# Optimization experiments

Hardware: AMD Instinct MI355X
Metric: run time of the kernel (lower is better)

Reference implementation:

```python
import jax, jax.numpy as jnp
import numpy as np

BETA = 1.0
EPS_MU = 1e-6
EPS_LOG = 1e-8
D_DIM = 2048
M_EVENTS = 16384
T_HORIZON = 100


def setup_inputs() -> dict:
    key = jax.random.key(0)
    k1, k2 = jax.random.split(key)
    # sorted event times in [0, T_HORIZON)
    t_events = jnp.sort(jax.random.uniform(k1, (M_EVENTS,), jnp.float32) * T_HORIZON)
    marks = jax.random.randint(k2, (M_EVENTS,), 0, D_DIM)  # int marks in {0..D-1}
    # learned params, init exactly as in torch module
    log_mu = jnp.full((D_DIM,), -3.0, jnp.float32)
    log_alpha = jnp.full((D_DIM, D_DIM), -4.0, jnp.float32)
    return {
        "t_events": t_events,
        "marks": marks,
        "T_max": T_HORIZON,
        "log_mu": log_mu,
        "log_alpha": log_alpha,
    }


def _loglik(t_events, log_mu, log_alpha, marks, T_max, beta=BETA):
    mu = jax.nn.softplus(log_mu) + EPS_MU          # [D]
    alpha = jax.nn.softplus(log_alpha)             # [D, D]
    D = mu.shape[0]
    # dt[0] = 0 so the first step leaves S (= zeros) untouched, matching the
    # torch loop which skips decay at n == 0.
    dt = jnp.concatenate([jnp.zeros((1,), t_events.dtype), jnp.diff(t_events)])  # [M]

    def step(S, xs):
        dt_n, d = xs
        S = jnp.exp(-beta * dt_n) * S              # exponential decay of state [D]
        lam_d = mu[d] + alpha[d] @ S               # intensity at event's mark
        S = S.at[d].add(1.0)                       # self-excitation bump
        return S, jnp.log(lam_d + EPS_LOG)

    _, log_lams = jax.lax.scan(step, jnp.zeros((D,), mu.dtype), (dt, marks))

    # compensator integral term
    T = jnp.asarray(T_max, t_events.dtype)
    one_minus_exp = 1.0 - jnp.exp(-beta * (T - t_events))          # [M]
    contrib = jax.ops.segment_sum(one_minus_exp, marks, num_segments=D)  # [D]
    integral = mu * T + alpha @ (contrib / beta)                   # [D]
    return log_lams.sum() - integral.sum()


def reference(t_events, marks, T_max, log_mu, log_alpha):
    return _loglik(t_events, log_mu, log_alpha, marks, T_max)
```

## Files before the change

### kernel.cpp

```cpp
#include <hip/hip_runtime.h>
#include <math.h>

#define D_DIM 2048
#define M_EV  16384
#define LCH   32
#define CCH   (M_EV / LCH)
#define SEG   32
#define NSEG  (CCH / SEG)
#define EPSEG (SEG * LCH)
#define BETA  1.0f
#define CPB   8

__device__ __forceinline__ float softplus_f(float x){
  float e = __expf(-fabsf(x));
  return fmaxf(x, 0.0f) + __logf(1.0f + e);
}

__device__ __forceinline__ unsigned short f2bf(float f){
  unsigned b = __float_as_uint(f);
  return (unsigned short)((b + 0x7FFFu + ((b >> 16) & 1u)) >> 16);
}
__device__ __forceinline__ float bf2f(unsigned short u){
  return __uint_as_float(((unsigned)u) << 16);
}

__device__ __forceinline__ float decode_T(const void* p){
  unsigned bits = *(const unsigned*)p;
  float fv = __uint_as_float(bits);
  return (fv >= 1e-3f && fv <= 1e7f) ? fv : (float)(int)bits;
}

__device__ __forceinline__ float wave_red(float v){
  #pragma unroll
  for (int o = 32; o > 0; o >>= 1) v += __shfl_down(v, o);
  return v;
}

__global__ __launch_bounds__(256) void k_prep(
    const float* __restrict__ t, const int* __restrict__ m,
    const float* __restrict__ log_mu, const void* Tp,
    float* __restrict__ muw, float* __restrict__ Cpart,
    float* __restrict__ acc)
{
  __shared__ float Cl[D_DIM];
  __shared__ float red[4];
  const int b = blockIdx.x, tid = threadIdx.x;
  if (b < 8){
    int j = b*256 + tid;
    float v = softplus_f(log_mu[j]) + 1e-6f;
    muw[j] = v;
    float s = wave_red(v);
    if ((tid & 63) == 0) red[tid >> 6] = s;
    __syncthreads();
    if (tid == 0) acc[8 + b] = (red[0]+red[1]) + (red[2]+red[3]);
  } else if (b < 8 + CPB){
    float4* Cl4 = (float4*)Cl;
    const float4 z = make_float4(0.f,0.f,0.f,0.f);
    Cl4[tid*2] = z; Cl4[tid*2 + 1] = z;
    __syncthreads();
    const float T = decode_T(Tp);
    #pragma unroll
    for (int k = 0; k < 8; ++k){
      int i = (b-8)*2048 + k*256 + tid;
      atomicAdd(&Cl[m[i]], 1.0f - __expf(-BETA * (T - t[i])));
    }
    __syncthreads();
    float4* Cp4 = (float4*)(Cpart + (size_t)(b-8) * D_DIM);
    Cp4[tid*2]     = Cl4[tid*2];
    Cp4[tid*2 + 1] = Cl4[tid*2 + 1];
  } else {
    if (tid < 8) acc[tid] = 0.f;
  }
}

__global__ __launch_bounds__(256) void k_scan_alpha(
    const float* __restrict__ t, const int* __restrict__ m,
    float* __restrict__ SL, float* __restrict__ Carry,
    const float* __restrict__ la, const float* __restrict__ Cpart,
    unsigned short* __restrict__ sA, float* __restrict__ acc)
{
  __shared__ float Stile[SEG * 256];
  __shared__ float tec[SEG];
  __shared__ float dch[SEG];
  const int b = blockIdx.x, tid = threadIdx.x;
  if (b < 128){
    const int seg = b >> 3, jb = b & 7;
    {
      float4* S4 = (float4*)Stile;
      const float4 z = make_float4(0.f,0.f,0.f,0.f);
      #pragma unroll
      for (int k = 0; k < 8; ++k) S4[k*256 + tid] = z;
    }
    if (tid < SEG){
      int c = seg*SEG + tid;
      if (c < CCH-1){
        float te = t[(c+1)*LCH];
        tec[tid] = te;
        dch[tid] = __expf(t[c*LCH] - te);
      } else {
        tec[tid] = 0.f;
        dch[tid] = 1.0f;
      }
    }
    __syncthreads();
    #pragma unroll
    for (int e = 0; e < 4; ++e){
      int il = e*256 + tid;
      int i  = seg*EPSEG + il;
      int cl = il >> 5;
      int c  = seg*SEG + cl;
      int mk = m[i] - jb*256;
      if (c < CCH-1 && (unsigned)mk < 256u)
        atomicAdd(&Stile[cl*256 + mk], __expf(t[i] - tec[cl]));
    }
    __syncthreads();
    const int col = jb*256 + tid;
    float u = 0.f;
    #pragma unroll 4
    for (int cl = 0; cl < SEG; ++cl){
      int c = seg*SEG + cl;
      SL[(size_t)c * D_DIM + col] = u;
      u = fmaf(dch[cl], u, Stile[cl*256 + tid]);
    }
    Carry[(size_t)seg * D_DIM + col] = u;
    return;
  }
  const int nthreads = 512*256;
  int atid = (b-128)*256 + tid;
  const float4* Cp4 = (const float4*)Cpart;
  const int cq = atid & 511;
  float4 cb = make_float4(0.f,0.f,0.f,0.f);
  #pragma unroll
  for (int r = 0; r < CPB; ++r){
    float4 v = Cp4[r*512 + cq];
    cb.x += v.x; cb.y += v.y; cb.z += v.z; cb.w += v.w;
  }
  const float4* la4 = (const float4*)la;
  ushort4* sA4 = (ushort4*)sA;
  float p = 0.f;
  #pragma unroll
  for (int u = 0; u < 8; ++u){
    int i4 = atid + u * nthreads;
    float4 x = la4[i4];
    float4 sp;
    sp.x = softplus_f(x.x); sp.y = softplus_f(x.y);
    sp.z = softplus_f(x.z); sp.w = softplus_f(x.w);
    ushort4 h;
    h.x = f2bf(sp.x); h.y = f2bf(sp.y); h.z = f2bf(sp.z); h.w = f2bf(sp.w);
    sA4[i4] = h;
    p = fmaf(sp.x, cb.x, p);
    p = fmaf(sp.y, cb.y, p);
    p = fmaf(sp.z, cb.z, p);
    p = fmaf(sp.w, cb.w, p);
  }
  float w = wave_red(p);
  int lane = tid & 63, wid = tid >> 6;
  if (lane == 0) Stile[wid] = w;
  __syncthreads();
  if (tid == 0) atomicAdd(&acc[1], Stile[0]+Stile[1]+Stile[2]+Stile[3]);
}

__global__ __launch_bounds__(512) void k_events(
    const float* __restrict__ t, const int* __restrict__ m,
    const unsigned short* __restrict__ sA, const float* __restrict__ muw,
    const float* __restrict__ SL, const float* __restrict__ Carry,
    float* __restrict__ acc, const void* Tp, float* __restrict__ out){
  __shared__ float S0[D_DIM];
  __shared__ float tl[LCH];
  __shared__ int   ml[LCH];
  __shared__ float wred[8];
  __shared__ float asg[16];
  const int tid = threadIdx.x;
  const int c = blockIdx.x;
  const int seg = c >> 5;

  if (tid < LCH){
    ml[tid] = m[c*LCH + tid];
    tl[tid] = t[c*LCH + tid];
  } else if (tid >= 64 && tid < 64 + NSEG - 1){
    int s = tid - 64;
    asg[s] = __expf(t[s*EPSEG] - t[(s+1)*EPSEG]);
  }
  __syncthreads();

  {
    const float cd = __expf(t[seg*EPSEG] - tl[0]);
    const float4 sv = *(const float4*)(SL + (size_t)c * D_DIM + tid*4);
    float4 e = {0.f, 0.f, 0.f, 0.f};
    float wgt = 1.f;
    for (int s = seg - 1; s >= 0; --s){
      const float4 cr = *(const float4*)(Carry + (size_t)s * D_DIM + tid*4);
      e.x = fmaf(cr.x, wgt, e.x); e.y = fmaf(cr.y, wgt, e.y);
      e.z = fmaf(cr.z, wgt, e.z); e.w = fmaf(cr.w, wgt, e.w);
      wgt *= asg[s];
    }
    float4 s;
    s.x = fmaf(e.x, cd, sv.x); s.y = fmaf(e.y, cd, sv.y);
    s.z = fmaf(e.z, cd, sv.z); s.w = fmaf(e.w, cd, sv.w);
    *(float4*)&S0[tid*4] = s;
  }
  __syncthreads();

  const int l = tid & 63, w = tid >> 6;
  const int l4 = l * 4;

  float4 s0[8];
  #pragma unroll
  for (int u = 0; u < 8; ++u) s0[u] = *(const float4*)&S0[u*256 + l4];

  const float t0 = tl[0];
  float lgw = 0.f;
  #pragma unroll
  for (int q = 0; q < 4; ++q){
    const int k = w*4 + q;
    const int d = ml[k];
    const unsigned short* row = sA + (size_t)d * D_DIM;
    float p = 0.f;
    #pragma unroll
    for (int u = 0; u < 8; ++u){
      ushort4 a = *(const ushort4*)(row + u*256 + l4);
      p = fmaf(bf2f(a.x), s0[u].x, p);
      p = fmaf(bf2f(a.y), s0[u].y, p);
      p = fmaf(bf2f(a.z), s0[u].z, p);
      p = fmaf(bf2f(a.w), s0[u].w, p);
    }
    const float tk = tl[k];
    float g = 0.f;
    if (l < k) g = bf2f(row[ml[l]]) * __expf(tl[l] - tk);
    p = fmaf(p, __expf(t0 - tk), g);
    float v = wave_red(p);
    if (l == 0) lgw += __logf(muw[d] + v + 1e-8f);
  }
  if (l == 0) wred[w] = lgw;
  __syncthreads();
  if (tid == 0){
    float lg = ((wred[0]+wred[1])+(wred[2]+wred[3]))
             + ((wred[4]+wred[5])+(wred[6]+wred[7]));
    atomicAdd(&acc[0], lg);
    __threadfence();
    unsigned old = atomicAdd((unsigned*)&acc[3], 1u);
    if (old == CCH - 1){
      float a0 = atomicAdd(&acc[0], 0.0f);
      float a1 = atomicAdd(&acc[1], 0.0f);
      float musum = 0.f;
      #pragma unroll
      for (int j = 8; j < 16; ++j) musum += atomicAdd(&acc[j], 0.0f);
      float T = decode_T(Tp);
      out[0] = a0 - (T * musum + a1 * (1.0f / BETA));
    }
  }
}

extern "C" void kernel_launch(void* const* d_in, const int* in_sizes, int n_in,
                              void* d_out, int out_size, void* d_ws, size_t ws_size,
                              hipStream_t stream) {
  const float* t_events  = (const float*)d_in[0];
  const int*   marks     = (const int*)  d_in[1];
  const void*  Tp        =               d_in[2];
  const float* log_mu    = (const float*)d_in[3];
  const float* log_alpha = (const float*)d_in[4];
  float* out = (float*)d_out;

  float* ws      = (float*)d_ws;
  float* SL      = ws;
  float* Carry   = SL + (size_t)CCH * D_DIM;
  float* muw     = Carry + (size_t)NSEG * D_DIM;
  float* Cpart   = muw + D_DIM;
  float* acc     = Cpart + (size_t)CPB * D_DIM;
  unsigned short* sA = (unsigned short*)(acc + 16);

  k_prep      <<<17, 256, 0, stream>>>(t_events, marks, log_mu, Tp,
                                       muw, Cpart, acc);
  k_scan_alpha<<<640, 256, 0, stream>>>(t_events, marks, SL, Carry,
                                        log_alpha, Cpart, sA, acc);
  k_events    <<<CCH, 512, 0, stream>>>(t_events, marks, sA, muw, SL, Carry,
                                        acc, Tp, out);
}
```

Measured before the change: 113.4 us.

## Recompute in-segment prefix state in LDS instead of materializing per-chunk SL

Drops the per-chunk prefix-state array SL, which was 512 × 2048 floats written by the scan kernel and read back by the event kernel. Each event block now rebuilds its within-segment state by scattering the earlier events of its segment into shared memory with atomics, decayed to the chunk start. The segment carries move into extra blocks of the prep kernel, so the former scan/alpha kernel shrinks to just the alpha softplus and reduction. This trades several megabytes of global traffic for up to about 1000 LDS atomics per event block, which can contend on repeated marks.

Result: no change. 112.7 us (-0.6%).

```diff
diff --git a/kernel.cpp b/kernel.cpp
--- a/kernel.cpp
+++ b/kernel.cpp
@@ -40,7 +40,7 @@
     const float* __restrict__ t, const int* __restrict__ m,
     const float* __restrict__ log_mu, const void* Tp,
     float* __restrict__ muw, float* __restrict__ Cpart,
-    float* __restrict__ acc)
+    float* __restrict__ Carry, float* __restrict__ acc)
 {
   __shared__ float Cl[D_DIM];
   __shared__ float red[4];
@@ -68,65 +68,34 @@
     float4* Cp4 = (float4*)(Cpart + (size_t)(b-8) * D_DIM);
     Cp4[tid*2]     = Cl4[tid*2];
     Cp4[tid*2 + 1] = Cl4[tid*2 + 1];
+  } else if (b < 31){
+    const int seg = b - 16;
+    float4* Cl4 = (float4*)Cl;
+    const float4 z = make_float4(0.f,0.f,0.f,0.f);
+    Cl4[tid*2] = z; Cl4[tid*2 + 1] = z;
+    __syncthreads();
+    const float te = t[(seg+1)*EPSEG];
+    #pragma unroll
+    for (int k = 0; k < 4; ++k){
+      int i = seg*EPSEG + k*256 + tid;
+      atomicAdd(&Cl[m[i]], __expf(t[i] - te));
+    }
+    __syncthreads();
+    float4* Cr4 = (float4*)(Carry + (size_t)seg * D_DIM);
+    Cr4[tid*2]     = Cl4[tid*2];
+    Cr4[tid*2 + 1] = Cl4[tid*2 + 1];
   } else {
     if (tid < 8) acc[tid] = 0.f;
   }
 }
 
-__global__ __launch_bounds__(256) void k_scan_alpha(
-    const float* __restrict__ t, const int* __restrict__ m,
-    float* __restrict__ SL, float* __restrict__ Carry,
+__global__ __launch_bounds__(256) void k_alpha(
     const float* __restrict__ la, const float* __restrict__ Cpart,
     unsigned short* __restrict__ sA, float* __restrict__ acc)
 {
-  __shared__ float Stile[SEG * 256];
-  __shared__ float tec[SEG];
-  __shared__ float dch[SEG];
   const int b = blockIdx.x, tid = threadIdx.x;
-  if (b < 128){
-    const int seg = b >> 3, jb = b & 7;
-    {
-      float4* S4 = (float4*)Stile;
-      const float4 z = make_float4(0.f,0.f,0.f,0.f);
-      #pragma unroll
-      for (int k = 0; k < 8; ++k) S4[k*256 + tid] = z;
-    }
-    if (tid < SEG){
-      int c = seg*SEG + tid;
-      if (c < CCH-1){
-        float te = t[(c+1)*LCH];
-        tec[tid] = te;
-        dch[tid] = __expf(t[c*LCH] - te);
-      } else {
-        tec[tid] = 0.f;
-        dch[tid] = 1.0f;
-      }
-    }
-    __syncthreads();
-    #pragma unroll
-    for (int e = 0; e < 4; ++e){
-      int il = e*256 + tid;
-      int i  = seg*EPSEG + il;
-      int cl = il >> 5;
-      int c  = seg*SEG + cl;
-      int mk = m[i] - jb*256;
-      if (c < CCH-1 && (unsigned)mk < 256u)
-        atomicAdd(&Stile[cl*256 + mk], __expf(t[i] - tec[cl]));
-    }
-    __syncthreads();
-    const int col = jb*256 + tid;
-    float u = 0.f;
-    #pragma unroll 4
-    for (int cl = 0; cl < SEG; ++cl){
-      int c = seg*SEG + cl;
-      SL[(size_t)c * D_DIM + col] = u;
-      u = fmaf(dch[cl], u, Stile[cl*256 + tid]);
-    }
-    Carry[(size_t)seg * D_DIM + col] = u;
-    return;
-  }
   const int nthreads = 512*256;
-  int atid = (b-128)*256 + tid;
+  int atid = b*256 + tid;
   const float4* Cp4 = (const float4*)Cpart;
   const int cq = atid & 511;
   float4 cb = make_float4(0.f,0.f,0.f,0.f);
@@ -153,18 +122,19 @@
     p = fmaf(sp.z, cb.z, p);
     p = fmaf(sp.w, cb.w, p);
   }
+  __shared__ float red[4];
   float w = wave_red(p);
   int lane = tid & 63, wid = tid >> 6;
-  if (lane == 0) Stile[wid] = w;
-  __syncthreads();
-  if (tid == 0) atomicAdd(&acc[1], Stile[0]+Stile[1]+Stile[2]+Stile[3]);
+  if (lane == 0) red[wid] = w;
+  __syncthreads();
+  if (tid == 0) atomicAdd(&acc[1], red[0]+red[1]+red[2]+red[3]);
 }
 
 __global__ __launch_bounds__(512) void k_events(
     const float* __restrict__ t, const int* __restrict__ m,
     const unsigned short* __restrict__ sA, const float* __restrict__ muw,
-    const float* __restrict__ SL, const float* __restrict__ Carry,
-    float* __restrict__ acc, const void* Tp, float* __restrict__ out){
+    const float* __restrict__ Carry, float* __restrict__ acc,
+    const void* Tp, float* __restrict__ out){
   __shared__ float S0[D_DIM];
   __shared__ float tl[LCH];
   __shared__ int   ml[LCH];
@@ -174,6 +144,7 @@
   const int c = blockIdx.x;
   const int seg = c >> 5;
 
+  *(float4*)&S0[tid*4] = make_float4(0.f,0.f,0.f,0.f);
   if (tid < LCH){
     ml[tid] = m[c*LCH + tid];
     tl[tid] = t[c*LCH + tid];
@@ -183,9 +154,16 @@
   }
   __syncthreads();
 
+  const float t0 = tl[0];
+  const int nev = (c & 31) * LCH;
+  for (int il = tid; il < nev; il += 512){
+    int i = seg*EPSEG + il;
+    atomicAdd(&S0[m[i]], __expf(t[i] - t0));
+  }
+  __syncthreads();
+
   {
-    const float cd = __expf(t[seg*EPSEG] - tl[0]);
-    const float4 sv = *(const float4*)(SL + (size_t)c * D_DIM + tid*4);
+    const float cd = __expf(t[seg*EPSEG] - t0);
     float4 e = {0.f, 0.f, 0.f, 0.f};
     float wgt = 1.f;
     for (int s = seg - 1; s >= 0; --s){
@@ -194,10 +172,10 @@
       e.z = fmaf(cr.z, wgt, e.z); e.w = fmaf(cr.w, wgt, e.w);
       wgt *= asg[s];
     }
-    float4 s;
-    s.x = fmaf(e.x, cd, sv.x); s.y = fmaf(e.y, cd, sv.y);
-    s.z = fmaf(e.z, cd, sv.z); s.w = fmaf(e.w, cd, sv.w);
-    *(float4*)&S0[tid*4] = s;
+    float4 sv = *(float4*)&S0[tid*4];
+    sv.x = fmaf(e.x, cd, sv.x); sv.y = fmaf(e.y, cd, sv.y);
+    sv.z = fmaf(e.z, cd, sv.z); sv.w = fmaf(e.w, cd, sv.w);
+    *(float4*)&S0[tid*4] = sv;
   }
   __syncthreads();
 
@@ -208,7 +186,6 @@
   #pragma unroll
   for (int u = 0; u < 8; ++u) s0[u] = *(const float4*)&S0[u*256 + l4];
 
-  const float t0 = tl[0];
   float lgw = 0.f;
   #pragma unroll
   for (int q = 0; q < 4; ++q){
@@ -262,17 +239,15 @@
   float* out = (float*)d_out;
 
   float* ws      = (float*)d_ws;
-  float* SL      = ws;
-  float* Carry   = SL + (size_t)CCH * D_DIM;
+  float* Carry   = ws;
   float* muw     = Carry + (size_t)NSEG * D_DIM;
   float* Cpart   = muw + D_DIM;
   float* acc     = Cpart + (size_t)CPB * D_DIM;
   unsigned short* sA = (unsigned short*)(acc + 16);
 
-  k_prep      <<<17, 256, 0, stream>>>(t_events, marks, log_mu, Tp,
-                                       muw, Cpart, acc);
-  k_scan_alpha<<<640, 256, 0, stream>>>(t_events, marks, SL, Carry,
-                                        log_alpha, Cpart, sA, acc);
-  k_events    <<<CCH, 512, 0, stream>>>(t_events, marks, sA, muw, SL, Carry,
-                                        acc, Tp, out);
-}
+  k_prep  <<<32, 256, 0, stream>>>(t_events, marks, log_mu, Tp,
+                                   muw, Cpart, Carry, acc);
+  k_alpha <<<512, 256, 0, stream>>>(log_alpha, Cpart, sA, acc);
+  k_events<<<CCH, 512, 0, stream>>>(t_events, marks, sA, muw, Carry,
+                                    acc, Tp, out);
+}
```
